# Kernel optimization log

Hardware: AMD Instinct MI355X
Metric: run time of the kernel (lower is better)

The kernel has to match this reference:

```python
import jax, jax.numpy as jnp
import numpy as np


def _normalize(x, axis=-1, eps=1e-12):
    n = jnp.linalg.norm(x, axis=axis, keepdims=True)
    return x / jnp.maximum(n, eps)


def _mlp(x, w1, b1, w2, b2):
    return jnp.maximum(x @ w1 + b1, 0.0) @ w2 + b2


def _quat_mul(a, b):
    # openfold (w, x, y, z) convention, Hamilton product
    aw, ax, ay, az = a[..., 0], a[..., 1], a[..., 2], a[..., 3]
    bw, bx, by, bz = b[..., 0], b[..., 1], b[..., 2], b[..., 3]
    return jnp.stack([
        aw * bw - ax * bx - ay * by - az * bz,
        aw * bx + ax * bw + ay * bz - az * by,
        aw * by - ax * bz + ay * bw + az * bx,
        aw * bz + ax * by - ay * bx + az * bw], axis=-1)


def _quat_rotate(q, v):
    # rotate vector v by unit quaternion q
    w = q[..., :1]
    u = q[..., 1:]
    t = 2.0 * jnp.cross(u, v)
    return v + w * t + jnp.cross(u, t)


def _conj(q):
    return q * jnp.asarray([1.0, -1.0, -1.0, -1.0], dtype=q.dtype)


def setup_inputs() -> dict:
    B, N, P, H, E, M = 2, 384, 128, 64, 32, 64
    key = jax.random.key(0)
    ks = iter(jax.random.split(key, 64))

    def nrm(shape):
        return jax.random.normal(next(ks), shape, dtype=jnp.float32)

    inp = {
        "frames_q": _normalize(nrm((B, N, 4))),
        "frames_x": nrm((B, N, 3)),
        "torsions": nrm((B, N, 7, 2)),
        "h": nrm((B, N, H)),
        "e": nrm((B, N, N, E)),
        "node_mask": jnp.ones((B, N), dtype=bool),
        "pocket_h": nrm((B, P, H)),
        "pocket_e": nrm((B, N, P, E)),
        "pocket_q": _normalize(nrm((B, P, 4))),
        "pocket_x": nrm((B, P, 3)),
        "pocket_mask": jnp.ones((B, P), dtype=bool),
    }
    # 2-layer MLPs with transition_size = 64
    for name, (fin, fout) in {"msg": (2 * H + E + 9, M), "feat": (H + M, H),
                              "tr": (M, 3), "qu": (M, 4), "to": (M, 14)}.items():
        inp[f"{name}_w1"] = nrm((fin, 64)) / np.sqrt(fin)
        inp[f"{name}_b1"] = nrm((64,)) * 0.01
        inp[f"{name}_w2"] = nrm((64, fout)) / np.sqrt(64)
        inp[f"{name}_b2"] = nrm((fout,)) * 0.01
    return inp


def reference(frames_q, frames_x, torsions, h, e, node_mask, pocket_h, pocket_e,
              pocket_q, pocket_x, pocket_mask,
              msg_w1, msg_b1, msg_w2, msg_b2,
              feat_w1, feat_b1, feat_w2, feat_b2,
              tr_w1, tr_b1, tr_w2, tr_b2,
              qu_w1, qu_b1, qu_w2, qu_b2,
              to_w1, to_b1, to_w2, to_b2):
    B, N, Hd = h.shape
    P = pocket_h.shape[-2]

    q_all = jnp.concatenate([frames_q, pocket_q], axis=-2)  # [B, N+P, 4]
    x_all = jnp.concatenate([frames_x, pocket_x], axis=-2)  # [B, N+P, 3]

    eye = jnp.eye(N, dtype=bool)
    mm = jnp.concatenate([
        node_mask[:, :, None] & node_mask[:, None, :] & ~eye,
        node_mask[:, :, None] & pocket_mask[:, None, :]], axis=-1)  # [B, N, N+P]

    vec = frames_x[:, :, None, :] - x_all[:, None, :, :]  # [B, N, N+P, 3]
    d2 = jnp.sum(vec * vec, axis=-1)                       # [B, N, N+P]
    qdot = jnp.abs(jnp.sum(frames_q[:, :, None, :] * q_all[:, None, :, :], axis=-1))

    # global -> local frame of node j applied to node i: R_j^T (x_i - t_j)
    qc = _conj(q_all)[:, None, :, :]                       # [B, 1, N+P, 4]
    local_x = _quat_rotate(qc, vec)                        # [B, N, N+P, 3]
    local_q = _quat_mul(qc, jnp.broadcast_to(frames_q[:, :, None, :], (B, N, N + P, 4)))

    feat = jnp.concatenate([
        jnp.broadcast_to(h[:, :, None, :], (B, N, N + P, Hd)),
        jnp.broadcast_to(jnp.concatenate([h, pocket_h], axis=-2)[:, None, :, :], (B, N, N + P, Hd)),
        jnp.concatenate([e, pocket_e], axis=-2),
        local_x, local_q, d2[..., None], qdot[..., None]], axis=-1)

    m = _mlp(feat, msg_w1, msg_b1, msg_w2, msg_b2) * mm[..., None]  # [B, N, N+P, M]
    msum = jnp.sum(m, axis=-2)                                      # [B, N, M]

    o = _mlp(jnp.concatenate([h, msum], axis=-1), feat_w1, feat_b1, feat_w2, feat_b2)

    dx = _mlp(m, tr_w1, tr_b1, tr_w2, tr_b2) * mm[..., None]        # [B, N, N+P, 3]

    ident = jnp.asarray([1.0, 0.0, 0.0, 0.0], dtype=frames_q.dtype)
    dq = _mlp(msum, qu_w1, qu_b1, qu_w2, qu_b2)
    dq = _normalize(jnp.where(node_mask[..., None], dq, ident))
    upd_q = _quat_mul(frames_q, dq)
    upd_q = _normalize(jnp.where(node_mask[..., None], upd_q, ident))

    qn_all = _normalize(q_all)
    gdx = jnp.sum(_quat_rotate(qn_all[:, None, :, :], dx), axis=-2)  # [B, N, 3]
    n_nb = (node_mask.sum(-1) + pocket_mask.sum(-1) - 1).astype(frames_x.dtype)
    upd_x = frames_x + gdx / n_nb[:, None, None]

    upd_torsions = _normalize(_mlp(msum, to_w1, to_b1, to_w2, to_b2).reshape(torsions.shape))

    return upd_q, upd_x, upd_torsions, o
```

## Files before the change

kernel.cpp:

```cpp
#include <hip/hip_runtime.h>
#include <math.h>

#define BB 2
#define NN 384
#define PP 128
#define HH 64
#define EE 32
#define NP 512
#define K1S 136
#define K2S 72

#define X_OFF (BB*NN*4)
#define T_OFF (X_OFF + BB*NN*3)
#define O_OFF (T_OFF + BB*NN*14)

using bf16x8 = __attribute__((ext_vector_type(8))) __bf16;
using f32x4  = __attribute__((ext_vector_type(4))) float;

__device__ __forceinline__ f32x4 MFMA(bf16x8 a, bf16x8 b, f32x4 c) {
  return __builtin_amdgcn_mfma_f32_16x16x32_bf16(a, b, c, 0, 0, 0);
}
__device__ __forceinline__ bf16x8 LDF(const __bf16* base, int off) {
  return *(const bf16x8*)(base + off);
}
__device__ __forceinline__ bf16x8 pack8(f32x4 lo, f32x4 hi) {
  bf16x8 r;
  r[0]=(__bf16)lo[0]; r[1]=(__bf16)lo[1]; r[2]=(__bf16)lo[2]; r[3]=(__bf16)lo[3];
  r[4]=(__bf16)hi[0]; r[5]=(__bf16)hi[1]; r[6]=(__bf16)hi[2]; r[7]=(__bf16)hi[3];
  return r;
}
__device__ __forceinline__ bf16x8 pack8v(float4 lo, float4 hi) {
  bf16x8 r;
  r[0]=(__bf16)lo.x; r[1]=(__bf16)lo.y; r[2]=(__bf16)lo.z; r[3]=(__bf16)lo.w;
  r[4]=(__bf16)hi.x; r[5]=(__bf16)hi.y; r[6]=(__bf16)hi.z; r[7]=(__bf16)hi.w;
  return r;
}
__device__ __forceinline__ int rowpos(int n) {
  const int t = (n>>5)*2 + ((n>>2)&1);
  const int q = ((n>>3)&3)*4 + (n&3);
  return t*16 + q;
}

__global__ __launch_bounds__(512, 2) void egnn_edge_swapped(
    const float* __restrict__ frames_q, const float* __restrict__ frames_x,
    const float* __restrict__ h, const float* __restrict__ e,
    const int* __restrict__ node_mask,
    const float* __restrict__ pocket_h, const float* __restrict__ pe,
    const float* __restrict__ pocket_q, const float* __restrict__ pocket_x,
    const int* __restrict__ pocket_mask,
    const float* __restrict__ w1, const float* __restrict__ b1,
    const float* __restrict__ w2, const float* __restrict__ b2,
    const float* __restrict__ tw1, const float* __restrict__ tb1,
    const float* __restrict__ tw2, const float* __restrict__ tb2,
    float* __restrict__ msum_ws, float* __restrict__ gdx_ws)
{
  __shared__ __align__(16) __bf16 s_w1p[64*K1S];
  __shared__ __align__(16) __bf16 s_w2p[64*K2S];
  __shared__ __align__(16) __bf16 s_tw1p[64*K2S];
  __shared__ __align__(16) __bf16 s_tw2p[16*K2S];
  __shared__ __align__(16) __bf16 s_geo[NP*16 + 8];
  __shared__ __align__(16) float s_qn[NP*4];
  __shared__ float s_maskf[NP];
  __shared__ float s_b2[64], s_tb1[64], s_tb2[4];
  __shared__ float s_msum[64], s_gdx[3];

  const int tid = threadIdx.x;
  const int b = blockIdx.x / NN, i = blockIdx.x % NN;

  for (int idx = tid; idx < 64*128; idx += 512) {
    const int n = idx & 63, k = idx >> 6;
    float v = 0.f;
    if      (k < 64)  v = w1[(64 + k)*64 + n];
    else if (k < 96)  v = w1[(128 + (k-64))*64 + n];
    else if (k < 105) v = w1[(160 + (k-96))*64 + n];
    if (k != 105) s_w1p[rowpos(n)*K1S + k] = (__bf16)v;
  }
  for (int idx = tid; idx < 64*64; idx += 512) {
    const int n = idx & 63, k = idx >> 6;
    s_w2p[rowpos(n)*K2S + k]  = (__bf16)w2[k*64 + n];
    s_tw1p[rowpos(n)*K2S + k] = (__bf16)tw1[k*64 + n];
  }
  for (int idx = tid; idx < 16*64; idx += 512) {
    const int row = idx >> 6, k = idx & 63;
    s_tw2p[row*K2S + k] = (__bf16)((row < 3) ? tw2[k*3 + row] : 0.f);
  }
  if (tid < 64) { s_b2[tid] = b2[tid]; s_tb1[tid] = tb1[tid]; s_msum[tid] = 0.f; }
  if (tid < 8)  s_geo[NP*16 + tid] = (__bf16)0.f;
  if (tid < 3)  { s_tb2[tid] = tb2[tid]; s_gdx[tid] = 0.f; }

  {
    const int n = tid >> 3, part = tid & 7;
    const float* hi = &h[(b*NN + i)*HH];
    float a = 0.f;
#pragma unroll
    for (int c = 0; c < 8; ++c) a = fmaf(hi[part*8 + c], w1[(part*8 + c)*64 + n], a);
    a += __shfl_xor(a, 1); a += __shfl_xor(a, 2); a += __shfl_xor(a, 4);
    if (part == 0) s_w1p[rowpos(n)*K1S + 105] = (__bf16)(a + b1[n]);
  }

  {
    const int j = tid;
    const int maski = node_mask[b*NN + i];
    const float qi0 = frames_q[(b*NN+i)*4+0], qi1 = frames_q[(b*NN+i)*4+1],
                qi2 = frames_q[(b*NN+i)*4+2], qi3 = frames_q[(b*NN+i)*4+3];
    const float xi0 = frames_x[(b*NN+i)*3+0], xi1 = frames_x[(b*NN+i)*3+1],
                xi2 = frames_x[(b*NN+i)*3+2];
    float qj0,qj1,qj2,qj3, xj0,xj1,xj2; int mj;
    if (j < NN) {
      const float4 q4 = *(const float4*)&frames_q[(b*NN+j)*4];
      qj0=q4.x; qj1=q4.y; qj2=q4.z; qj3=q4.w;
      xj0=frames_x[(b*NN+j)*3+0]; xj1=frames_x[(b*NN+j)*3+1]; xj2=frames_x[(b*NN+j)*3+2];
      mj = (node_mask[b*NN+j] != 0) && (j != i);
    } else {
      const int jp = j - NN;
      const float4 q4 = *(const float4*)&pocket_q[(b*PP+jp)*4];
      qj0=q4.x; qj1=q4.y; qj2=q4.z; qj3=q4.w;
      xj0=pocket_x[(b*PP+jp)*3+0]; xj1=pocket_x[(b*PP+jp)*3+1]; xj2=pocket_x[(b*PP+jp)*3+2];
      mj = (pocket_mask[b*PP+jp] != 0);
    }
    const float v0 = xi0 - xj0, v1 = xi1 - xj1, v2 = xi2 - xj2;
    const float d2 = v0*v0 + v1*v1 + v2*v2;
    const float qdot = fabsf(qi0*qj0 + qi1*qj1 + qi2*qj2 + qi3*qj3);
    const float cw = qj0, cx = -qj1, cy = -qj2, cz = -qj3;
    const float t0 = 2.f*(cy*v2 - cz*v1);
    const float t1 = 2.f*(cz*v0 - cx*v2);
    const float t2 = 2.f*(cx*v1 - cy*v0);
    const float lx0 = v0 + cw*t0 + (cy*t2 - cz*t1);
    const float lx1 = v1 + cw*t1 + (cz*t0 - cx*t2);
    const float lx2 = v2 + cw*t2 + (cx*t1 - cy*t0);
    const float lq0 = cw*qi0 - cx*qi1 - cy*qi2 - cz*qi3;
    const float lq1 = cw*qi1 + cx*qi0 + cy*qi3 - cz*qi2;
    const float lq2 = cw*qi2 - cx*qi3 + cy*qi0 + cz*qi1;
    const float lq3 = cw*qi3 + cx*qi2 - cy*qi1 + cz*qi0;
    __bf16* g = &s_geo[j*16];
    g[0]=(__bf16)lx0; g[1]=(__bf16)lx1; g[2]=(__bf16)lx2; g[3]=(__bf16)lq0;
    g[4]=(__bf16)lq1; g[5]=(__bf16)lq2; g[6]=(__bf16)lq3; g[7]=(__bf16)d2;
    g[8]=(__bf16)qdot; g[9]=(__bf16)1.f;
    g[10]=(__bf16)0.f; g[11]=(__bf16)0.f; g[12]=(__bf16)0.f;
    g[13]=(__bf16)0.f; g[14]=(__bf16)0.f; g[15]=(__bf16)0.f;
    s_maskf[j] = (maski && mj) ? 1.f : 0.f;
    const float inv = 1.f / fmaxf(sqrtf(qj0*qj0 + qj1*qj1 + qj2*qj2 + qj3*qj3), 1e-12f);
    float4* qn = (float4*)&s_qn[j*4];
    *qn = make_float4(qj0*inv, qj1*inv, qj2*inv, qj3*inv);
  }
  __syncthreads();

  const int wv = tid >> 6, lane = tid & 63;
  const int l15 = lane & 15, lg = lane >> 4;

  bf16x8 tw2f[2];
  tw2f[0] = *(const bf16x8*)&s_tw2p[l15*K2S +  0 + lg*8];
  tw2f[1] = *(const bf16x8*)&s_tw2p[l15*K2S + 32 + lg*8];

  float b2r[16], tb1r[16];
#pragma unroll
  for (int t2 = 0; t2 < 4; ++t2)
#pragma unroll
    for (int r = 0; r < 4; ++r) {
      const int n2 = (t2>>1)*32 + lg*8 + (t2&1)*4 + r;
      b2r[t2*4 + r]  = s_b2[n2];
      tb1r[t2*4 + r] = s_tb1[n2];
    }
  const float tb2r0 = s_tb2[0], tb2r1 = s_tb2[1], tb2r2 = s_tb2[2];

  float msacc[16];
#pragma unroll
  for (int v = 0; v < 16; ++v) msacc[v] = 0.f;
  float gx0 = 0.f, gx1 = 0.f, gx2 = 0.f;

  const int o1base = l15*K1S + lg*8;
  const int o2base = l15*K2S + lg*8;

#define LOADSTRIP(S, H0_,H1_,H2_,H3_,E0_,E1_) do {                          \
    const int jbase_ = wv*64 + (S)*16;                                      \
    const int j_ = jbase_ + l15;                                            \
    const float *hj_, *ej_;                                                 \
    if (jbase_ < NN) {                                                      \
      hj_ = &h[(b*NN + j_)*HH];                                             \
      ej_ = &e[((b*NN + i)*NN + j_)*EE];                                    \
    } else {                                                                \
      const int jp_ = j_ - NN;                                              \
      hj_ = &pocket_h[(b*PP + jp_)*HH];                                     \
      ej_ = &pe[((b*NN + i)*PP + jp_)*EE];                                  \
    }                                                                       \
    H0_ = *(const float4*)&hj_[lg*8];                                       \
    H1_ = *(const float4*)&hj_[lg*8 + 4];                                   \
    H2_ = *(const float4*)&hj_[32 + lg*8];                                  \
    H3_ = *(const float4*)&hj_[32 + lg*8 + 4];                              \
    E0_ = *(const float4*)&ej_[lg*8];                                       \
    E1_ = *(const float4*)&ej_[lg*8 + 4];                                   \
  } while (0)

  float4 cH0, cH1, cH2, cH3, cE0, cE1;
  float4 nH0, nH1, nH2, nH3, nE0, nE1;
  LOADSTRIP(0, cH0, cH1, cH2, cH3, cE0, cE1);

#pragma unroll
  for (int s = 0; s < 4; ++s) {
    if (s < 3) LOADSTRIP(s+1, nH0, nH1, nH2, nH3, nE0, nE1);

    int o1 = o1base; asm volatile("" : "+v"(o1));
    int o2 = o2base; asm volatile("" : "+v"(o2));

    const int j = wv*64 + s*16 + l15;
    const float mask_f = s_maskf[j];

    const bf16x8 bf0 = pack8v(cH0, cH1);
    const bf16x8 bf1 = pack8v(cH2, cH3);
    const bf16x8 bf2 = pack8v(cE0, cE1);
    const bf16x8 bf3 = *(const bf16x8*)&s_geo[(lg < 2) ? (j*16 + lg*8) : NP*16];

    const f32x4 zero4 = {0.f, 0.f, 0.f, 0.f};
    f32x4 a0 = MFMA(LDF(s_w1p, o1 + 0*16*K1S +  0), bf0, zero4);
    a0 = MFMA(LDF(s_w1p, o1 + 0*16*K1S + 32), bf1, a0);
    a0 = MFMA(LDF(s_w1p, o1 + 0*16*K1S + 64), bf2, a0);
    a0 = MFMA(LDF(s_w1p, o1 + 0*16*K1S + 96), bf3, a0);
    f32x4 a1 = MFMA(LDF(s_w1p, o1 + 1*16*K1S +  0), bf0, zero4);
    a1 = MFMA(LDF(s_w1p, o1 + 1*16*K1S + 32), bf1, a1);
    a1 = MFMA(LDF(s_w1p, o1 + 1*16*K1S + 64), bf2, a1);
    a1 = MFMA(LDF(s_w1p, o1 + 1*16*K1S + 96), bf3, a1);
#pragma unroll
    for (int r = 0; r < 4; ++r) { a0[r] = fmaxf(a0[r], 0.f); a1[r] = fmaxf(a1[r], 0.f); }
    const bf16x8 hb0 = pack8(a0, a1);
    f32x4 a2 = MFMA(LDF(s_w1p, o1 + 2*16*K1S +  0), bf0, zero4);
    a2 = MFMA(LDF(s_w1p, o1 + 2*16*K1S + 32), bf1, a2);
    a2 = MFMA(LDF(s_w1p, o1 + 2*16*K1S + 64), bf2, a2);
    a2 = MFMA(LDF(s_w1p, o1 + 2*16*K1S + 96), bf3, a2);
    f32x4 a3 = MFMA(LDF(s_w1p, o1 + 3*16*K1S +  0), bf0, zero4);
    a3 = MFMA(LDF(s_w1p, o1 + 3*16*K1S + 32), bf1, a3);
    a3 = MFMA(LDF(s_w1p, o1 + 3*16*K1S + 64), bf2, a3);
    a3 = MFMA(LDF(s_w1p, o1 + 3*16*K1S + 96), bf3, a3);
#pragma unroll
    for (int r = 0; r < 4; ++r) { a2[r] = fmaxf(a2[r], 0.f); a3[r] = fmaxf(a3[r], 0.f); }
    const bf16x8 hb1 = pack8(a2, a3);

    f32x4 c0 = MFMA(LDF(s_w2p, o2 + 0*16*K2S +  0), hb0, zero4);
    c0 = MFMA(LDF(s_w2p, o2 + 0*16*K2S + 32), hb1, c0);
    f32x4 c1 = MFMA(LDF(s_w2p, o2 + 1*16*K2S +  0), hb0, zero4);
    c1 = MFMA(LDF(s_w2p, o2 + 1*16*K2S + 32), hb1, c1);
#pragma unroll
    for (int r = 0; r < 4; ++r) {
      c0[r] = (c0[r] + b2r[0*4+r]) * mask_f;  msacc[0*4+r] += c0[r];
      c1[r] = (c1[r] + b2r[1*4+r]) * mask_f;  msacc[1*4+r] += c1[r];
    }
    const bf16x8 mb0 = pack8(c0, c1);
    f32x4 c2 = MFMA(LDF(s_w2p, o2 + 2*16*K2S +  0), hb0, zero4);
    c2 = MFMA(LDF(s_w2p, o2 + 2*16*K2S + 32), hb1, c2);
    f32x4 c3 = MFMA(LDF(s_w2p, o2 + 3*16*K2S +  0), hb0, zero4);
    c3 = MFMA(LDF(s_w2p, o2 + 3*16*K2S + 32), hb1, c3);
#pragma unroll
    for (int r = 0; r < 4; ++r) {
      c2[r] = (c2[r] + b2r[2*4+r]) * mask_f;  msacc[2*4+r] += c2[r];
      c3[r] = (c3[r] + b2r[3*4+r]) * mask_f;  msacc[3*4+r] += c3[r];
    }
    const bf16x8 mb1 = pack8(c2, c3);

    f32x4 d0 = MFMA(LDF(s_tw1p, o2 + 0*16*K2S +  0), mb0, zero4);
    d0 = MFMA(LDF(s_tw1p, o2 + 0*16*K2S + 32), mb1, d0);
    f32x4 d1 = MFMA(LDF(s_tw1p, o2 + 1*16*K2S +  0), mb0, zero4);
    d1 = MFMA(LDF(s_tw1p, o2 + 1*16*K2S + 32), mb1, d1);
#pragma unroll
    for (int r = 0; r < 4; ++r) {
      d0[r] = fmaxf(d0[r] + tb1r[0*4+r], 0.f);
      d1[r] = fmaxf(d1[r] + tb1r[1*4+r], 0.f);
    }
    const bf16x8 thb0 = pack8(d0, d1);
    f32x4 d2f = MFMA(LDF(s_tw1p, o2 + 2*16*K2S +  0), mb0, zero4);
    d2f = MFMA(LDF(s_tw1p, o2 + 2*16*K2S + 32), mb1, d2f);
    f32x4 d3 = MFMA(LDF(s_tw1p, o2 + 3*16*K2S +  0), mb0, zero4);
    d3 = MFMA(LDF(s_tw1p, o2 + 3*16*K2S + 32), mb1, d3);
#pragma unroll
    for (int r = 0; r < 4; ++r) {
      d2f[r] = fmaxf(d2f[r] + tb1r[2*4+r], 0.f);
      d3[r]  = fmaxf(d3[r]  + tb1r[3*4+r], 0.f);
    }
    const bf16x8 thb1 = pack8(d2f, d3);

    f32x4 dacc = MFMA(tw2f[0], thb0, zero4);
    dacc = MFMA(tw2f[1], thb1, dacc);

    if (lg == 0) {
      const float dx0 = (dacc[0] + tb2r0) * mask_f;
      const float dx1 = (dacc[1] + tb2r1) * mask_f;
      const float dx2 = (dacc[2] + tb2r2) * mask_f;
      const float4 qn = *(const float4*)&s_qn[j*4];
      const float w = qn.x, ux = qn.y, uy = qn.z, uz = qn.w;
      const float r0 = 2.f*(uy*dx2 - uz*dx1);
      const float r1 = 2.f*(uz*dx0 - ux*dx2);
      const float r2 = 2.f*(ux*dx1 - uy*dx0);
      gx0 += dx0 + w*r0 + (uy*r2 - uz*r1);
      gx1 += dx1 + w*r1 + (uz*r0 - ux*r2);
      gx2 += dx2 + w*r2 + (ux*r1 - uy*r0);
    }

    if (s < 3) {
      cH0 = nH0; cH1 = nH1; cH2 = nH2; cH3 = nH3; cE0 = nE0; cE1 = nE1;
    }
  }
#undef LOADSTRIP

#pragma unroll
  for (int v = 0; v < 16; ++v) {
    float x = msacc[v];
    x += __shfl_xor(x, 1); x += __shfl_xor(x, 2);
    x += __shfl_xor(x, 4); x += __shfl_xor(x, 8);
    if (l15 == 0) {
      const int n2 = (v>>3)*32 + lg*8 + ((v>>2)&1)*4 + (v&3);
      atomicAdd(&s_msum[n2], x);
    }
  }
  {
    float v0 = (lg == 0) ? gx0 : 0.f;
    float v1 = (lg == 0) ? gx1 : 0.f;
    float v2 = (lg == 0) ? gx2 : 0.f;
#pragma unroll
    for (int sft = 1; sft < 64; sft <<= 1) {
      v0 += __shfl_xor(v0, sft); v1 += __shfl_xor(v1, sft); v2 += __shfl_xor(v2, sft);
    }
    if (lane == 0) { atomicAdd(&s_gdx[0], v0); atomicAdd(&s_gdx[1], v1); atomicAdd(&s_gdx[2], v2); }
  }
  __syncthreads();
  if (tid < 64) msum_ws[(b*NN + i)*64 + tid] = s_msum[tid];
  if (tid >= 64 && tid < 67) gdx_ws[(b*NN + i)*3 + (tid - 64)] = s_gdx[tid - 64];
}

__global__ __launch_bounds__(64) void egnn_node_kernel(
    const float* __restrict__ frames_q, const float* __restrict__ frames_x,
    const float* __restrict__ h,
    const int* __restrict__ node_mask, const int* __restrict__ pocket_mask,
    const float* __restrict__ fw1, const float* __restrict__ fb1,
    const float* __restrict__ fw2, const float* __restrict__ fb2,
    const float* __restrict__ qw1, const float* __restrict__ qb1,
    const float* __restrict__ qw2, const float* __restrict__ qb2,
    const float* __restrict__ tow1, const float* __restrict__ tob1,
    const float* __restrict__ tow2, const float* __restrict__ tob2,
    const float* __restrict__ msum_ws, const float* __restrict__ gdx_ws,
    float* __restrict__ out)
{
  const int t  = threadIdx.x;
  const int bi = blockIdx.x;
  const int b = bi / NN, i = bi % NN;
  __shared__ float s_h[64], s_ms[64], s_hid[64], s_tmp[16];

  s_h[t]  = h[(b*NN+i)*HH + t];
  s_ms[t] = msum_ws[(b*NN+i)*64 + t];

  int cnt = 0;
  for (int k = t; k < NN; k += 64) cnt += (node_mask[b*NN+k] != 0);
  for (int k = t; k < PP; k += 64) cnt += (pocket_mask[b*PP+k] != 0);
  cnt += __shfl_xor(cnt,1); cnt += __shfl_xor(cnt,2); cnt += __shfl_xor(cnt,4);
  cnt += __shfl_xor(cnt,8); cnt += __shfl_xor(cnt,16); cnt += __shfl_xor(cnt,32);
  const float n_nb = (float)(cnt - 1);

  __syncthreads();
  float a = fb1[t];
  for (int k = 0; k < 64; ++k) a = fmaf(s_h[k],  fw1[k*64 + t], a);
  for (int k = 0; k < 64; ++k) a = fmaf(s_ms[k], fw1[(64+k)*64 + t], a);
  s_hid[t] = fmaxf(a, 0.f);
  __syncthreads();
  float ov = fb2[t];
  for (int k = 0; k < 64; ++k) ov = fmaf(s_hid[k], fw2[k*64 + t], ov);
  out[O_OFF + (b*NN+i)*64 + t] = ov;

  __syncthreads();
  float aq = qb1[t];
  for (int k = 0; k < 64; ++k) aq = fmaf(s_ms[k], qw1[k*64 + t], aq);
  s_hid[t] = fmaxf(aq, 0.f);
  __syncthreads();
  if (t < 4) {
    float d = qb2[t];
    for (int k = 0; k < 64; ++k) d = fmaf(s_hid[k], qw2[k*4 + t], d);
    s_tmp[t] = d;
  }
  __syncthreads();
  if (t == 0) {
    const int mi = node_mask[b*NN+i];
    float d0,d1,d2,d3;
    if (mi) { d0=s_tmp[0]; d1=s_tmp[1]; d2=s_tmp[2]; d3=s_tmp[3]; }
    else    { d0=1.f; d1=0.f; d2=0.f; d3=0.f; }
    float nrm = fmaxf(sqrtf(d0*d0+d1*d1+d2*d2+d3*d3), 1e-12f);
    d0/=nrm; d1/=nrm; d2/=nrm; d3/=nrm;
    const float q0=frames_q[(b*NN+i)*4+0], q1=frames_q[(b*NN+i)*4+1],
                q2=frames_q[(b*NN+i)*4+2], q3=frames_q[(b*NN+i)*4+3];
    float u0 = q0*d0 - q1*d1 - q2*d2 - q3*d3;
    float u1 = q0*d1 + q1*d0 + q2*d3 - q3*d2;
    float u2 = q0*d2 - q1*d3 + q2*d0 + q3*d1;
    float u3 = q0*d3 + q1*d2 - q2*d1 + q3*d0;
    if (!mi) { u0=1.f; u1=0.f; u2=0.f; u3=0.f; }
    float nrm2 = fmaxf(sqrtf(u0*u0+u1*u1+u2*u2+u3*u3), 1e-12f);
    out[(b*NN+i)*4+0]=u0/nrm2; out[(b*NN+i)*4+1]=u1/nrm2;
    out[(b*NN+i)*4+2]=u2/nrm2; out[(b*NN+i)*4+3]=u3/nrm2;
  }
  if (t < 3) {
    out[X_OFF + (b*NN+i)*3 + t] = frames_x[(b*NN+i)*3+t] + gdx_ws[(b*NN+i)*3+t] / n_nb;
  }

  __syncthreads();
  float at = tob1[t];
  for (int k = 0; k < 64; ++k) at = fmaf(s_ms[k], tow1[k*64 + t], at);
  s_hid[t] = fmaxf(at, 0.f);
  __syncthreads();
  if (t < 14) {
    float v = tob2[t];
    for (int k = 0; k < 64; ++k) v = fmaf(s_hid[k], tow2[k*14 + t], v);
    s_tmp[t] = v;
  }
  __syncthreads();
  if (t < 14) {
    const int p = t & ~1;
    const float a0 = s_tmp[p], a1 = s_tmp[p+1];
    const float nrm = fmaxf(sqrtf(a0*a0 + a1*a1), 1e-12f);
    out[T_OFF + (b*NN+i)*14 + t] = s_tmp[t] / nrm;
  }
}

extern "C" void kernel_launch(void* const* d_in, const int* in_sizes, int n_in,
                              void* d_out, int out_size, void* d_ws, size_t ws_size,
                              hipStream_t stream) {
  const float* frames_q    = (const float*)d_in[0];
  const float* frames_x    = (const float*)d_in[1];
  const float* h           = (const float*)d_in[3];
  const float* e           = (const float*)d_in[4];
  const int*   node_mask   = (const int*)d_in[5];
  const float* pocket_h    = (const float*)d_in[6];
  const float* pocket_e    = (const float*)d_in[7];
  const float* pocket_q    = (const float*)d_in[8];
  const float* pocket_x    = (const float*)d_in[9];
  const int*   pocket_mask = (const int*)d_in[10];
  const float* msg_w1 = (const float*)d_in[11];
  const float* msg_b1 = (const float*)d_in[12];
  const float* msg_w2 = (const float*)d_in[13];
  const float* msg_b2 = (const float*)d_in[14];
  const float* feat_w1 = (const float*)d_in[15];
  const float* feat_b1 = (const float*)d_in[16];
  const float* feat_w2 = (const float*)d_in[17];
  const float* feat_b2 = (const float*)d_in[18];
  const float* tr_w1 = (const float*)d_in[19];
  const float* tr_b1 = (const float*)d_in[20];
  const float* tr_w2 = (const float*)d_in[21];
  const float* tr_b2 = (const float*)d_in[22];
  const float* qu_w1 = (const float*)d_in[23];
  const float* qu_b1 = (const float*)d_in[24];
  const float* qu_w2 = (const float*)d_in[25];
  const float* qu_b2 = (const float*)d_in[26];
  const float* to_w1 = (const float*)d_in[27];
  const float* to_b1 = (const float*)d_in[28];
  const float* to_w2 = (const float*)d_in[29];
  const float* to_b2 = (const float*)d_in[30];

  float* out = (float*)d_out;
  float* msum_ws = (float*)d_ws;
  float* gdx_ws  = msum_ws + BB*NN*64;

  egnn_edge_swapped<<<dim3(BB*NN), dim3(512), 0, stream>>>(
      frames_q, frames_x, h, e, node_mask,
      pocket_h, pocket_e, pocket_q, pocket_x, pocket_mask,
      msg_w1, msg_b1, msg_w2, msg_b2,
      tr_w1, tr_b1, tr_w2, tr_b2,
      msum_ws, gdx_ws);

  egnn_node_kernel<<<dim3(BB*NN), dim3(64), 0, stream>>>(
      frames_q, frames_x, h, node_mask, pocket_mask,
      feat_w1, feat_b1, feat_w2, feat_b2,
      qu_w1, qu_b1, qu_w2, qu_b2,
      to_w1, to_b1, to_w2, to_b2,
      msum_ws, gdx_ws, out);
}
```

Before: 65.92 us.

## Make edge kernel persistent with 1024-thread blocks looping over three nodes

The edge kernel now launches 256 blocks of 1024 threads, and each block processes three query nodes in turn. The packed bf16 weights are converted and staged into shared memory once per block instead of once per node. Each wave now handles 32 neighbours in two strips, without the register double-buffered prefetch of the next strip. Bias values are read from shared memory as vectors instead of being held in 32 registers. The extra __syncthreads per node and the loss of load prefetching may expose global-memory latency, and one block per CU reduces the ability to overlap work across blocks.

```diff
diff --git a/kernel.cpp b/kernel.cpp
--- a/kernel.cpp
+++ b/kernel.cpp
@@ -41,7 +41,7 @@
   return t*16 + q;
 }
 
-__global__ __launch_bounds__(512, 2) void egnn_edge_swapped(
+__global__ __launch_bounds__(1024, 1) void egnn_edge_persist(
     const float* __restrict__ frames_q, const float* __restrict__ frames_x,
     const float* __restrict__ h, const float* __restrict__ e,
     const int* __restrict__ node_mask,
@@ -61,13 +61,13 @@
   __shared__ __align__(16) __bf16 s_geo[NP*16 + 8];
   __shared__ __align__(16) float s_qn[NP*4];
   __shared__ float s_maskf[NP];
-  __shared__ float s_b2[64], s_tb1[64], s_tb2[4];
+  __shared__ __align__(16) float s_b2[64], s_tb1[64];
+  __shared__ float s_tb2[4];
   __shared__ float s_msum[64], s_gdx[3];
 
   const int tid = threadIdx.x;
-  const int b = blockIdx.x / NN, i = blockIdx.x % NN;
-
-  for (int idx = tid; idx < 64*128; idx += 512) {
+
+  for (int idx = tid; idx < 64*128; idx += 1024) {
     const int n = idx & 63, k = idx >> 6;
     float v = 0.f;
     if      (k < 64)  v = w1[(64 + k)*64 + n];
@@ -75,74 +75,18 @@
     else if (k < 105) v = w1[(160 + (k-96))*64 + n];
     if (k != 105) s_w1p[rowpos(n)*K1S + k] = (__bf16)v;
   }
-  for (int idx = tid; idx < 64*64; idx += 512) {
+  for (int idx = tid; idx < 64*64; idx += 1024) {
     const int n = idx & 63, k = idx >> 6;
     s_w2p[rowpos(n)*K2S + k]  = (__bf16)w2[k*64 + n];
     s_tw1p[rowpos(n)*K2S + k] = (__bf16)tw1[k*64 + n];
   }
-  for (int idx = tid; idx < 16*64; idx += 512) {
+  for (int idx = tid; idx < 16*64; idx += 1024) {
     const int row = idx >> 6, k = idx & 63;
     s_tw2p[row*K2S + k] = (__bf16)((row < 3) ? tw2[k*3 + row] : 0.f);
   }
-  if (tid < 64) { s_b2[tid] = b2[tid]; s_tb1[tid] = tb1[tid]; s_msum[tid] = 0.f; }
+  if (tid < 64) { s_b2[tid] = b2[tid]; s_tb1[tid] = tb1[tid]; }
   if (tid < 8)  s_geo[NP*16 + tid] = (__bf16)0.f;
-  if (tid < 3)  { s_tb2[tid] = tb2[tid]; s_gdx[tid] = 0.f; }
-
-  {
-    const int n = tid >> 3, part = tid & 7;
-    const float* hi = &h[(b*NN + i)*HH];
-    float a = 0.f;
-#pragma unroll
-    for (int c = 0; c < 8; ++c) a = fmaf(hi[part*8 + c], w1[(part*8 + c)*64 + n], a);
-    a += __shfl_xor(a, 1); a += __shfl_xor(a, 2); a += __shfl_xor(a, 4);
-    if (part == 0) s_w1p[rowpos(n)*K1S + 105] = (__bf16)(a + b1[n]);
-  }
-
-  {
-    const int j = tid;
-    const int maski = node_mask[b*NN + i];
-    const float qi0 = frames_q[(b*NN+i)*4+0], qi1 = frames_q[(b*NN+i)*4+1],
-                qi2 = frames_q[(b*NN+i)*4+2], qi3 = frames_q[(b*NN+i)*4+3];
-    const float xi0 = frames_x[(b*NN+i)*3+0], xi1 = frames_x[(b*NN+i)*3+1],
-                xi2 = frames_x[(b*NN+i)*3+2];
-    float qj0,qj1,qj2,qj3, xj0,xj1,xj2; int mj;
-    if (j < NN) {
-      const float4 q4 = *(const float4*)&frames_q[(b*NN+j)*4];
-      qj0=q4.x; qj1=q4.y; qj2=q4.z; qj3=q4.w;
-      xj0=frames_x[(b*NN+j)*3+0]; xj1=frames_x[(b*NN+j)*3+1]; xj2=frames_x[(b*NN+j)*3+2];
-      mj = (node_mask[b*NN+j] != 0) && (j != i);
-    } else {
-      const int jp = j - NN;
-      const float4 q4 = *(const float4*)&pocket_q[(b*PP+jp)*4];
-      qj0=q4.x; qj1=q4.y; qj2=q4.z; qj3=q4.w;
-      xj0=pocket_x[(b*PP+jp)*3+0]; xj1=pocket_x[(b*PP+jp)*3+1]; xj2=pocket_x[(b*PP+jp)*3+2];
-      mj = (pocket_mask[b*PP+jp] != 0);
-    }
-    const float v0 = xi0 - xj0, v1 = xi1 - xj1, v2 = xi2 - xj2;
-    const float d2 = v0*v0 + v1*v1 + v2*v2;
-    const float qdot = fabsf(qi0*qj0 + qi1*qj1 + qi2*qj2 + qi3*qj3);
-    const float cw = qj0, cx = -qj1, cy = -qj2, cz = -qj3;
-    const float t0 = 2.f*(cy*v2 - cz*v1);
-    const float t1 = 2.f*(cz*v0 - cx*v2);
-    const float t2 = 2.f*(cx*v1 - cy*v0);
-    const float lx0 = v0 + cw*t0 + (cy*t2 - cz*t1);
-    const float lx1 = v1 + cw*t1 + (cz*t0 - cx*t2);
-    const float lx2 = v2 + cw*t2 + (cx*t1 - cy*t0);
-    const float lq0 = cw*qi0 - cx*qi1 - cy*qi2 - cz*qi3;
-    const float lq1 = cw*qi1 + cx*qi0 + cy*qi3 - cz*qi2;
-    const float lq2 = cw*qi2 - cx*qi3 + cy*qi0 + cz*qi1;
-    const float lq3 = cw*qi3 + cx*qi2 - cy*qi1 + cz*qi0;
-    __bf16* g = &s_geo[j*16];
-    g[0]=(__bf16)lx0; g[1]=(__bf16)lx1; g[2]=(__bf16)lx2; g[3]=(__bf16)lq0;
-    g[4]=(__bf16)lq1; g[5]=(__bf16)lq2; g[6]=(__bf16)lq3; g[7]=(__bf16)d2;
-    g[8]=(__bf16)qdot; g[9]=(__bf16)1.f;
-    g[10]=(__bf16)0.f; g[11]=(__bf16)0.f; g[12]=(__bf16)0.f;
-    g[13]=(__bf16)0.f; g[14]=(__bf16)0.f; g[15]=(__bf16)0.f;
-    s_maskf[j] = (maski && mj) ? 1.f : 0.f;
-    const float inv = 1.f / fmaxf(sqrtf(qj0*qj0 + qj1*qj1 + qj2*qj2 + qj3*qj3), 1e-12f);
-    float4* qn = (float4*)&s_qn[j*4];
-    *qn = make_float4(qj0*inv, qj1*inv, qj2*inv, qj3*inv);
-  }
+  if (tid < 3)  s_tb2[tid] = tb2[tid];
   __syncthreads();
 
   const int wv = tid >> 6, lane = tid & 63;
@@ -151,31 +95,17 @@
   bf16x8 tw2f[2];
   tw2f[0] = *(const bf16x8*)&s_tw2p[l15*K2S +  0 + lg*8];
   tw2f[1] = *(const bf16x8*)&s_tw2p[l15*K2S + 32 + lg*8];
-
-  float b2r[16], tb1r[16];
-#pragma unroll
-  for (int t2 = 0; t2 < 4; ++t2)
-#pragma unroll
-    for (int r = 0; r < 4; ++r) {
-      const int n2 = (t2>>1)*32 + lg*8 + (t2&1)*4 + r;
-      b2r[t2*4 + r]  = s_b2[n2];
-      tb1r[t2*4 + r] = s_tb1[n2];
-    }
   const float tb2r0 = s_tb2[0], tb2r1 = s_tb2[1], tb2r2 = s_tb2[2];
-
-  float msacc[16];
-#pragma unroll
-  for (int v = 0; v < 16; ++v) msacc[v] = 0.f;
-  float gx0 = 0.f, gx1 = 0.f, gx2 = 0.f;
 
   const int o1base = l15*K1S + lg*8;
   const int o2base = l15*K2S + lg*8;
-
-#define LOADSTRIP(S, H0_,H1_,H2_,H3_,E0_,E1_) do {                          \
-    const int jbase_ = wv*64 + (S)*16;                                      \
-    const int j_ = jbase_ + l15;                                            \
+  const int obbase = lg*8;
+
+#define LOADSTRIP(JB0, H0_,H1_,H2_,H3_,E0_,E1_) do {                        \
+    const int jb_ = (JB0);                                                  \
+    const int j_ = jb_ + l15;                                               \
     const float *hj_, *ej_;                                                 \
-    if (jbase_ < NN) {                                                      \
+    if (jb_ < NN) {                                                         \
       hj_ = &h[(b*NN + j_)*HH];                                             \
       ej_ = &e[((b*NN + i)*NN + j_)*EE];                                    \
     } else {                                                                \
@@ -191,137 +121,221 @@
     E1_ = *(const float4*)&ej_[lg*8 + 4];                                   \
   } while (0)
 
-  float4 cH0, cH1, cH2, cH3, cE0, cE1;
-  float4 nH0, nH1, nH2, nH3, nE0, nE1;
-  LOADSTRIP(0, cH0, cH1, cH2, cH3, cE0, cE1);
-
-#pragma unroll
-  for (int s = 0; s < 4; ++s) {
-    if (s < 3) LOADSTRIP(s+1, nH0, nH1, nH2, nH3, nE0, nE1);
-
-    int o1 = o1base; asm volatile("" : "+v"(o1));
-    int o2 = o2base; asm volatile("" : "+v"(o2));
-
-    const int j = wv*64 + s*16 + l15;
-    const float mask_f = s_maskf[j];
-
-    const bf16x8 bf0 = pack8v(cH0, cH1);
-    const bf16x8 bf1 = pack8v(cH2, cH3);
-    const bf16x8 bf2 = pack8v(cE0, cE1);
-    const bf16x8 bf3 = *(const bf16x8*)&s_geo[(lg < 2) ? (j*16 + lg*8) : NP*16];
-
-    const f32x4 zero4 = {0.f, 0.f, 0.f, 0.f};
-    f32x4 a0 = MFMA(LDF(s_w1p, o1 + 0*16*K1S +  0), bf0, zero4);
-    a0 = MFMA(LDF(s_w1p, o1 + 0*16*K1S + 32), bf1, a0);
-    a0 = MFMA(LDF(s_w1p, o1 + 0*16*K1S + 64), bf2, a0);
-    a0 = MFMA(LDF(s_w1p, o1 + 0*16*K1S + 96), bf3, a0);
-    f32x4 a1 = MFMA(LDF(s_w1p, o1 + 1*16*K1S +  0), bf0, zero4);
-    a1 = MFMA(LDF(s_w1p, o1 + 1*16*K1S + 32), bf1, a1);
-    a1 = MFMA(LDF(s_w1p, o1 + 1*16*K1S + 64), bf2, a1);
-    a1 = MFMA(LDF(s_w1p, o1 + 1*16*K1S + 96), bf3, a1);
-#pragma unroll
-    for (int r = 0; r < 4; ++r) { a0[r] = fmaxf(a0[r], 0.f); a1[r] = fmaxf(a1[r], 0.f); }
-    const bf16x8 hb0 = pack8(a0, a1);
-    f32x4 a2 = MFMA(LDF(s_w1p, o1 + 2*16*K1S +  0), bf0, zero4);
-    a2 = MFMA(LDF(s_w1p, o1 + 2*16*K1S + 32), bf1, a2);
-    a2 = MFMA(LDF(s_w1p, o1 + 2*16*K1S + 64), bf2, a2);
-    a2 = MFMA(LDF(s_w1p, o1 + 2*16*K1S + 96), bf3, a2);
-    f32x4 a3 = MFMA(LDF(s_w1p, o1 + 3*16*K1S +  0), bf0, zero4);
-    a3 = MFMA(LDF(s_w1p, o1 + 3*16*K1S + 32), bf1, a3);
-    a3 = MFMA(LDF(s_w1p, o1 + 3*16*K1S + 64), bf2, a3);
-    a3 = MFMA(LDF(s_w1p, o1 + 3*16*K1S + 96), bf3, a3);
-#pragma unroll
-    for (int r = 0; r < 4; ++r) { a2[r] = fmaxf(a2[r], 0.f); a3[r] = fmaxf(a3[r], 0.f); }
-    const bf16x8 hb1 = pack8(a2, a3);
-
-    f32x4 c0 = MFMA(LDF(s_w2p, o2 + 0*16*K2S +  0), hb0, zero4);
-    c0 = MFMA(LDF(s_w2p, o2 + 0*16*K2S + 32), hb1, c0);
-    f32x4 c1 = MFMA(LDF(s_w2p, o2 + 1*16*K2S +  0), hb0, zero4);
-    c1 = MFMA(LDF(s_w2p, o2 + 1*16*K2S + 32), hb1, c1);
-#pragma unroll
-    for (int r = 0; r < 4; ++r) {
-      c0[r] = (c0[r] + b2r[0*4+r]) * mask_f;  msacc[0*4+r] += c0[r];
-      c1[r] = (c1[r] + b2r[1*4+r]) * mask_f;  msacc[1*4+r] += c1[r];
+#pragma unroll 1
+  for (int rep = 0; rep < 3; ++rep) {
+    const int ni = (int)blockIdx.x + rep*256;
+    const int b = ni / NN, i = ni % NN;
+
+    __syncthreads();
+    if (tid < 64) s_msum[tid] = 0.f;
+    if (tid < 3)  s_gdx[tid] = 0.f;
+
+    {
+      const int n = tid >> 4, part = tid & 15;
+      const float* hi = &h[(b*NN + i)*HH];
+      float a = 0.f;
+#pragma unroll
+      for (int c = 0; c < 4; ++c) a = fmaf(hi[part*4 + c], w1[(part*4 + c)*64 + n], a);
+      a += __shfl_xor(a, 1); a += __shfl_xor(a, 2);
+      a += __shfl_xor(a, 4); a += __shfl_xor(a, 8);
+      if (part == 0) s_w1p[rowpos(n)*K1S + 105] = (__bf16)(a + b1[n]);
     }
-    const bf16x8 mb0 = pack8(c0, c1);
-    f32x4 c2 = MFMA(LDF(s_w2p, o2 + 2*16*K2S +  0), hb0, zero4);
-    c2 = MFMA(LDF(s_w2p, o2 + 2*16*K2S + 32), hb1, c2);
-    f32x4 c3 = MFMA(LDF(s_w2p, o2 + 3*16*K2S +  0), hb0, zero4);
-    c3 = MFMA(LDF(s_w2p, o2 + 3*16*K2S + 32), hb1, c3);
-#pragma unroll
-    for (int r = 0; r < 4; ++r) {
-      c2[r] = (c2[r] + b2r[2*4+r]) * mask_f;  msacc[2*4+r] += c2[r];
-      c3[r] = (c3[r] + b2r[3*4+r]) * mask_f;  msacc[3*4+r] += c3[r];
+
+    if (tid < NP) {
+      const int j = tid;
+      const int maski = node_mask[b*NN + i];
+      const float qi0 = frames_q[(b*NN+i)*4+0], qi1 = frames_q[(b*NN+i)*4+1],
+                  qi2 = frames_q[(b*NN+i)*4+2], qi3 = frames_q[(b*NN+i)*4+3];
+      const float xi0 = frames_x[(b*NN+i)*3+0], xi1 = frames_x[(b*NN+i)*3+1],
+                  xi2 = frames_x[(b*NN+i)*3+2];
+      float qj0,qj1,qj2,qj3, xj0,xj1,xj2; int mj;
+      if (j < NN) {
+        const float4 q4 = *(const float4*)&frames_q[(b*NN+j)*4];
+        qj0=q4.x; qj1=q4.y; qj2=q4.z; qj3=q4.w;
+        xj0=frames_x[(b*NN+j)*3+0]; xj1=frames_x[(b*NN+j)*3+1]; xj2=frames_x[(b*NN+j)*3+2];
+        mj = (node_mask[b*NN+j] != 0) && (j != i);
+      } else {
+        const int jp = j - NN;
+        const float4 q4 = *(const float4*)&pocket_q[(b*PP+jp)*4];
+        qj0=q4.x; qj1=q4.y; qj2=q4.z; qj3=q4.w;
+        xj0=pocket_x[(b*PP+jp)*3+0]; xj1=pocket_x[(b*PP+jp)*3+1]; xj2=pocket_x[(b*PP+jp)*3+2];
+        mj = (pocket_mask[b*PP+jp] != 0);
+      }
+      const float v0 = xi0 - xj0, v1 = xi1 - xj1, v2 = xi2 - xj2;
+      const float d2 = v0*v0 + v1*v1 + v2*v2;
+      const float qdot = fabsf(qi0*qj0 + qi1*qj1 + qi2*qj2 + qi3*qj3);
+      const float cw = qj0, cx = -qj1, cy = -qj2, cz = -qj3;
+      const float t0 = 2.f*(cy*v2 - cz*v1);
+      const float t1 = 2.f*(cz*v0 - cx*v2);
+      const float t2 = 2.f*(cx*v1 - cy*v0);
+      const float lx0 = v0 + cw*t0 + (cy*t2 - cz*t1);
+      const float lx1 = v1 + cw*t1 + (cz*t0 - cx*t2);
+      const float lx2 = v2 + cw*t2 + (cx*t1 - cy*t0);
+      const float lq0 = cw*qi0 - cx*qi1 - cy*qi2 - cz*qi3;
+      const float lq1 = cw*qi1 + cx*qi0 + cy*qi3 - cz*qi2;
+      const float lq2 = cw*qi2 - cx*qi3 + cy*qi0 + cz*qi1;
+      const float lq3 = cw*qi3 + cx*qi2 - cy*qi1 + cz*qi0;
+      __bf16* g = &s_geo[j*16];
+      g[0]=(__bf16)lx0; g[1]=(__bf16)lx1; g[2]=(__bf16)lx2; g[3]=(__bf16)lq0;
+      g[4]=(__bf16)lq1; g[5]=(__bf16)lq2; g[6]=(__bf16)lq3; g[7]=(__bf16)d2;
+      g[8]=(__bf16)qdot; g[9]=(__bf16)1.f;
+      g[10]=(__bf16)0.f; g[11]=(__bf16)0.f; g[12]=(__bf16)0.f;
+      g[13]=(__bf16)0.f; g[14]=(__bf16)0.f; g[15]=(__bf16)0.f;
+      s_maskf[j] = (maski && mj) ? 1.f : 0.f;
+      const float inv = 1.f / fmaxf(sqrtf(qj0*qj0 + qj1*qj1 + qj2*qj2 + qj3*qj3), 1e-12f);
+      float4* qn = (float4*)&s_qn[j*4];
+      *qn = make_float4(qj0*inv, qj1*inv, qj2*inv, qj3*inv);
     }
-    const bf16x8 mb1 = pack8(c2, c3);
-
-    f32x4 d0 = MFMA(LDF(s_tw1p, o2 + 0*16*K2S +  0), mb0, zero4);
-    d0 = MFMA(LDF(s_tw1p, o2 + 0*16*K2S + 32), mb1, d0);
-    f32x4 d1 = MFMA(LDF(s_tw1p, o2 + 1*16*K2S +  0), mb0, zero4);
-    d1 = MFMA(LDF(s_tw1p, o2 + 1*16*K2S + 32), mb1, d1);
-#pragma unroll
-    for (int r = 0; r < 4; ++r) {
-      d0[r] = fmaxf(d0[r] + tb1r[0*4+r], 0.f);
-      d1[r] = fmaxf(d1[r] + tb1r[1*4+r], 0.f);
+    __syncthreads();
+
+    float msacc[16];
+#pragma unroll
+    for (int v = 0; v < 16; ++v) msacc[v] = 0.f;
+    float gx0 = 0.f, gx1 = 0.f, gx2 = 0.f;
+
+#pragma unroll 1
+    for (int ss = 0; ss < 2; ++ss) {
+      int o1 = o1base; asm volatile("" : "+v"(o1));
+      int o2 = o2base; asm volatile("" : "+v"(o2));
+      int ob = obbase; asm volatile("" : "+v"(ob));
+
+      const int jb = wv*32 + ss*16;
+      const int j = jb + l15;
+
+      float4 h0,h1,h2,h3,e0,e1;
+      LOADSTRIP(jb, h0,h1,h2,h3,e0,e1);
+      const float mask_f = s_maskf[j];
+
+      const bf16x8 bf0 = pack8v(h0, h1);
+      const bf16x8 bf1 = pack8v(h2, h3);
+      const bf16x8 bf2 = pack8v(e0, e1);
+      const bf16x8 bf3 = *(const bf16x8*)&s_geo[(lg < 2) ? (j*16 + lg*8) : NP*16];
+
+      const f32x4 zero4 = {0.f, 0.f, 0.f, 0.f};
+      f32x4 a0 = MFMA(LDF(s_w1p, o1 + 0*16*K1S +  0), bf0, zero4);
+      a0 = MFMA(LDF(s_w1p, o1 + 0*16*K1S + 32), bf1, a0);
+      a0 = MFMA(LDF(s_w1p, o1 + 0*16*K1S + 64), bf2, a0);
+      a0 = MFMA(LDF(s_w1p, o1 + 0*16*K1S + 96), bf3, a0);
+      f32x4 a1 = MFMA(LDF(s_w1p, o1 + 1*16*K1S +  0), bf0, zero4);
+      a1 = MFMA(LDF(s_w1p, o1 + 1*16*K1S + 32), bf1, a1);
+      a1 = MFMA(LDF(s_w1p, o1 + 1*16*K1S + 64), bf2, a1);
+      a1 = MFMA(LDF(s_w1p, o1 + 1*16*K1S + 96), bf3, a1);
+#pragma unroll
+      for (int r = 0; r < 4; ++r) { a0[r] = fmaxf(a0[r], 0.f); a1[r] = fmaxf(a1[r], 0.f); }
+      const bf16x8 hb0 = pack8(a0, a1);
+      f32x4 a2 = MFMA(LDF(s_w1p, o1 + 2*16*K1S +  0), bf0, zero4);
+      a2 = MFMA(LDF(s_w1p, o1 + 2*16*K1S + 32), bf1, a2);
+      a2 = MFMA(LDF(s_w1p, o1 + 2*16*K1S + 64), bf2, a2);
+      a2 = MFMA(LDF(s_w1p, o1 + 2*16*K1S + 96), bf3, a2);
+      f32x4 a3 = MFMA(LDF(s_w1p, o1 + 3*16*K1S +  0), bf0, zero4);
+      a3 = MFMA(LDF(s_w1p, o1 + 3*16*K1S + 32), bf1, a3);
+      a3 = MFMA(LDF(s_w1p, o1 + 3*16*K1S + 64), bf2, a3);
+      a3 = MFMA(LDF(s_w1p, o1 + 3*16*K1S + 96), bf3, a3);
+#pragma unroll
+      for (int r = 0; r < 4; ++r) { a2[r] = fmaxf(a2[r], 0.f); a3[r] = fmaxf(a3[r], 0.f); }
+      const bf16x8 hb1 = pack8(a2, a3);
+
+      f32x4 c0 = MFMA(LDF(s_w2p, o2 + 0*16*K2S +  0), hb0, zero4);
+      c0 = MFMA(LDF(s_w2p, o2 + 0*16*K2S + 32), hb1, c0);
+      f32x4 c1 = MFMA(LDF(s_w2p, o2 + 1*16*K2S +  0), hb0, zero4);
+      c1 = MFMA(LDF(s_w2p, o2 + 1*16*K2S + 32), hb1, c1);
+      {
+        const f32x4 bb0 = *(const f32x4*)&s_b2[ob + 0];
+        const f32x4 bb1 = *(const f32x4*)&s_b2[ob + 4];
+#pragma unroll
+        for (int r = 0; r < 4; ++r) {
+          c0[r] = (c0[r] + bb0[r]) * mask_f;  msacc[0*4+r] += c0[r];
+          c1[r] = (c1[r] + bb1[r]) * mask_f;  msacc[1*4+r] += c1[r];
+        }
+      }
+      const bf16x8 mb0 = pack8(c0, c1);
+      f32x4 c2 = MFMA(LDF(s_w2p, o2 + 2*16*K2S +  0), hb0, zero4);
+      c2 = MFMA(LDF(s_w2p, o2 + 2*16*K2S + 32), hb1, c2);
+      f32x4 c3 = MFMA(LDF(s_w2p, o2 + 3*16*K2S +  0), hb0, zero4);
+      c3 = MFMA(LDF(s_w2p, o2 + 3*16*K2S + 32), hb1, c3);
+      {
+        const f32x4 bb2 = *(const f32x4*)&s_b2[ob + 32];
+        const f32x4 bb3 = *(const f32x4*)&s_b2[ob + 36];
+#pragma unroll
+        for (int r = 0; r < 4; ++r) {
+          c2[r] = (c2[r] + bb2[r]) * mask_f;  msacc[2*4+r] += c2[r];
+          c3[r] = (c3[r] + bb3[r]) * mask_f;  msacc[3*4+r] += c3[r];
+        }
+      }
+      const bf16x8 mb1 = pack8(c2, c3);
+
+      f32x4 d0 = MFMA(LDF(s_tw1p, o2 + 0*16*K2S +  0), mb0, zero4);
+      d0 = MFMA(LDF(s_tw1p, o2 + 0*16*K2S + 32), mb1, d0);
+      f32x4 d1 = MFMA(LDF(s_tw1p, o2 + 1*16*K2S +  0), mb0, zero4);
+      d1 = MFMA(LDF(s_tw1p, o2 + 1*16*K2S + 32), mb1, d1);
+      {
+        const f32x4 tb0 = *(const f32x4*)&s_tb1[ob + 0];
+        const f32x4 tb1v = *(const f32x4*)&s_tb1[ob + 4];
+#pragma unroll
+        for (int r = 0; r < 4; ++r) {
+          d0[r] = fmaxf(d0[r] + tb0[r], 0.f);
+          d1[r] = fmaxf(d1[r] + tb1v[r], 0.f);
+        }
+      }
+      const bf16x8 thb0 = pack8(d0, d1);
+      f32x4 d2f = MFMA(LDF(s_tw1p, o2 + 2*16*K2S +  0), mb0, zero4);
+      d2f = MFMA(LDF(s_tw1p, o2 + 2*16*K2S + 32), mb1, d2f);
+      f32x4 d3 = MFMA(LDF(s_tw1p, o2 + 3*16*K2S +  0), mb0, zero4);
+      d3 = MFMA(LDF(s_tw1p, o2 + 3*16*K2S + 32), mb1, d3);
+      {
+        const f32x4 tb2v = *(const f32x4*)&s_tb1[ob + 32];
+        const f32x4 tb3v = *(const f32x4*)&s_tb1[ob + 36];
+#pragma unroll
+        for (int r = 0; r < 4; ++r) {
+          d2f[r] = fmaxf(d2f[r] + tb2v[r], 0.f);
+          d3[r]  = fmaxf(d3[r]  + tb3v[r], 0.f);
+        }
+      }
+      const bf16x8 thb1 = pack8(d2f, d3);
+
+      f32x4 dacc = MFMA(tw2f[0], thb0, zero4);
+      dacc = MFMA(tw2f[1], thb1, dacc);
+
+      if (lg == 0) {
+        const float dx0 = (dacc[0] + tb2r0) * mask_f;
+        const float dx1 = (dacc[1] + tb2r1) * mask_f;
+        const float dx2 = (dacc[2] + tb2r2) * mask_f;
+        const float4 qn = *(const float4*)&s_qn[j*4];
+        const float w = qn.x, ux = qn.y, uy = qn.z, uz = qn.w;
+        const float r0 = 2.f*(uy*dx2 - uz*dx1);
+        const float r1 = 2.f*(uz*dx0 - ux*dx2);
+        const float r2 = 2.f*(ux*dx1 - uy*dx0);
+        gx0 += dx0 + w*r0 + (uy*r2 - uz*r1);
+        gx1 += dx1 + w*r1 + (uz*r0 - ux*r2);
+        gx2 += dx2 + w*r2 + (ux*r1 - uy*r0);
+      }
     }
-    const bf16x8 thb0 = pack8(d0, d1);
-    f32x4 d2f = MFMA(LDF(s_tw1p, o2 + 2*16*K2S +  0), mb0, zero4);
-    d2f = MFMA(LDF(s_tw1p, o2 + 2*16*K2S + 32), mb1, d2f);
-    f32x4 d3 = MFMA(LDF(s_tw1p, o2 + 3*16*K2S +  0), mb0, zero4);
-    d3 = MFMA(LDF(s_tw1p, o2 + 3*16*K2S + 32), mb1, d3);
-#pragma unroll
-    for (int r = 0; r < 4; ++r) {
-      d2f[r] = fmaxf(d2f[r] + tb1r[2*4+r], 0.f);
-      d3[r]  = fmaxf(d3[r]  + tb1r[3*4+r], 0.f);
+
+#pragma unroll
+    for (int v = 0; v < 16; ++v) {
+      float x = msacc[v];
+      x += __shfl_xor(x, 1); x += __shfl_xor(x, 2);
+      x += __shfl_xor(x, 4); x += __shfl_xor(x, 8);
+      if (l15 == 0) {
+        const int n2 = (v>>3)*32 + lg*8 + ((v>>2)&1)*4 + (v&3);
+        atomicAdd(&s_msum[n2], x);
+      }
     }
-    const bf16x8 thb1 = pack8(d2f, d3);
-
-    f32x4 dacc = MFMA(tw2f[0], thb0, zero4);
-    dacc = MFMA(tw2f[1], thb1, dacc);
-
-    if (lg == 0) {
-      const float dx0 = (dacc[0] + tb2r0) * mask_f;
-      const float dx1 = (dacc[1] + tb2r1) * mask_f;
-      const float dx2 = (dacc[2] + tb2r2) * mask_f;
-      const float4 qn = *(const float4*)&s_qn[j*4];
-      const float w = qn.x, ux = qn.y, uy = qn.z, uz = qn.w;
-      const float r0 = 2.f*(uy*dx2 - uz*dx1);
-      const float r1 = 2.f*(uz*dx0 - ux*dx2);
-      const float r2 = 2.f*(ux*dx1 - uy*dx0);
-      gx0 += dx0 + w*r0 + (uy*r2 - uz*r1);
-      gx1 += dx1 + w*r1 + (uz*r0 - ux*r2);
-      gx2 += dx2 + w*r2 + (ux*r1 - uy*r0);
+    {
+      float v0 = (lg == 0) ? gx0 : 0.f;
+      float v1 = (lg == 0) ? gx1 : 0.f;
+      float v2 = (lg == 0) ? gx2 : 0.f;
+#pragma unroll
+      for (int sft = 1; sft < 64; sft <<= 1) {
+        v0 += __shfl_xor(v0, sft); v1 += __shfl_xor(v1, sft); v2 += __shfl_xor(v2, sft);
+      }
+      if (lane == 0) { atomicAdd(&s_gdx[0], v0); atomicAdd(&s_gdx[1], v1); atomicAdd(&s_gdx[2], v2); }
     }
-
-    if (s < 3) {
-      cH0 = nH0; cH1 = nH1; cH2 = nH2; cH3 = nH3; cE0 = nE0; cE1 = nE1;
-    }
+    __syncthreads();
+    if (tid < 64) msum_ws[ni*64 + tid] = s_msum[tid];
+    if (tid >= 64 && tid < 67) gdx_ws[ni*3 + (tid - 64)] = s_gdx[tid - 64];
   }
 #undef LOADSTRIP
-
-#pragma unroll
-  for (int v = 0; v < 16; ++v) {
-    float x = msacc[v];
-    x += __shfl_xor(x, 1); x += __shfl_xor(x, 2);
-    x += __shfl_xor(x, 4); x += __shfl_xor(x, 8);
-    if (l15 == 0) {
-      const int n2 = (v>>3)*32 + lg*8 + ((v>>2)&1)*4 + (v&3);
-      atomicAdd(&s_msum[n2], x);
-    }
-  }
-  {
-    float v0 = (lg == 0) ? gx0 : 0.f;
-    float v1 = (lg == 0) ? gx1 : 0.f;
-    float v2 = (lg == 0) ? gx2 : 0.f;
-#pragma unroll
-    for (int sft = 1; sft < 64; sft <<= 1) {
-      v0 += __shfl_xor(v0, sft); v1 += __shfl_xor(v1, sft); v2 += __shfl_xor(v2, sft);
-    }
-    if (lane == 0) { atomicAdd(&s_gdx[0], v0); atomicAdd(&s_gdx[1], v1); atomicAdd(&s_gdx[2], v2); }
-  }
-  __syncthreads();
-  if (tid < 64) msum_ws[(b*NN + i)*64 + tid] = s_msum[tid];
-  if (tid >= 64 && tid < 67) gdx_ws[(b*NN + i)*3 + (tid - 64)] = s_gdx[tid - 64];
 }
 
 __global__ __launch_bounds__(64) void egnn_node_kernel(
@@ -452,7 +466,7 @@
   float* msum_ws = (float*)d_ws;
   float* gdx_ws  = msum_ws + BB*NN*64;
 
-  egnn_edge_swapped<<<dim3(BB*NN), dim3(512), 0, stream>>>(
+  egnn_edge_persist<<<dim3(256), dim3(1024), 0, stream>>>(
       frames_q, frames_x, h, e, node_mask,
       pocket_h, pocket_e, pocket_q, pocket_x, pocket_mask,
       msg_w1, msg_b1, msg_w2, msg_b2,
```

Result: faster. 59.74 us, median of 2 (-9.4%).
